# Optimization experiments

Measured on AMD Instinct MI355X. Metric: run time of the kernel, lower is better.

## Reference

```python
import jax, jax.numpy as jnp
import numpy as np

N_NODES = 50000
NEG_SLOPE = 0.2


def _gat_layer(x, src, dst, W, att_src, att_dst, bias, concat):
    # x: [N, F_in]; W: [F_in, H*D]; att_*: [H, D]; bias: [H*D] or [D]
    H, D = att_src.shape
    N = x.shape[0]
    h = (x @ W).reshape(N, H, D)                       # [N, H, D]
    a_s = jnp.einsum('nhd,hd->nh', h, att_src)         # [N, H]
    a_d = jnp.einsum('nhd,hd->nh', h, att_dst)
    e = a_s[src] + a_d[dst]                            # [E, H]
    e = jnp.where(e > 0, e, NEG_SLOPE * e)             # LeakyReLU(0.2)
    # segment softmax over incoming edges of each target node
    e_max = jax.ops.segment_max(e, dst, num_segments=N)
    ex = jnp.exp(e - e_max[dst])
    denom = jax.ops.segment_sum(ex, dst, num_segments=N)
    alpha = ex / denom[dst]                            # [E, H]
    msg = h[src] * alpha[:, :, None]                   # [E, H, D]
    out = jax.ops.segment_sum(msg, dst, num_segments=N)  # [N, H, D]
    if concat:
        out = out.reshape(N, H * D)
    else:
        out = out.mean(axis=1)
    return out + bias


def _forward(x, edge_index, W1, att_src1, att_dst1, b1, W2, att_src2, att_dst2, b2):
    N = x.shape[0]
    loop = jnp.arange(N, dtype=edge_index.dtype)
    src = jnp.concatenate([edge_index[0], loop])       # add self-loops (PyG default)
    dst = jnp.concatenate([edge_index[1], loop])
    h = _gat_layer(x, src, dst, W1, att_src1, att_dst1, b1, concat=True)
    h = jax.nn.elu(h)
    h = _gat_layer(h, src, dst, W2, att_src2, att_dst2, b2, concat=False)
    return jax.nn.log_softmax(h, axis=-1)


def setup_inputs() -> dict:
    key = jax.random.key(0)
    ks = jax.random.split(key, 12)
    N, E, F_in, F_out, H, D = N_NODES, 1600000, 128, 64, 8, 32
    glorot = lambda k, shp: jax.random.normal(k, shp, jnp.float32) * np.sqrt(2.0 / (shp[0] + shp[-1]))
    return {
        'x': jax.random.normal(ks[0], (N, F_in), jnp.float32),
        'edge_index': jax.random.randint(ks[1], (2, E), 0, N, jnp.int64),
        'W1': glorot(ks[2], (F_in, H * D)),
        'att_src1': glorot(ks[3], (H, D)),
        'att_dst1': glorot(ks[4], (H, D)),
        'b1': jnp.zeros((H * D,), jnp.float32),
        'W2': glorot(ks[5], (H * D, F_out)),
        'att_src2': glorot(ks[6], (1, F_out)),
        'att_dst2': glorot(ks[7], (1, F_out)),
        'b2': jnp.zeros((F_out,), jnp.float32),
    }


def reference(x, edge_index, W1, att_src1, att_dst1, b1, W2, att_src2, att_dst2, b2):
    return _forward(x, edge_index, W1, att_src1, att_dst1, b1, W2, att_src2, att_dst2, b2)
```

## Files before the change

### kernel.cpp

```cpp
#include <hip/hip_runtime.h>
#include <hip/hip_bf16.h>
#include <math.h>


#define FIN 128
#define C1 256
#define NH 8
#define HD 32
#define C2 64
#define CH1 64

typedef float floatx2 __attribute__((ext_vector_type(2)));
typedef short bf16x8 __attribute__((ext_vector_type(8)));
typedef float f32x4 __attribute__((ext_vector_type(4)));

__device__ __forceinline__ float blo(unsigned u) { return __uint_as_float(u << 16); }
__device__ __forceinline__ float bhi(unsigned u) { return __uint_as_float(u & 0xffff0000u); }
__device__ __forceinline__ unsigned pkbf(float a, float b) {
    unsigned ua = __float_as_uint(a), ub = __float_as_uint(b);
    ua += 0x7fff + ((ua >> 16) & 1);
    ub += 0x7fff + ((ub >> 16) & 1);
    return (ua >> 16) | (ub & 0xffff0000u);
}

__global__ void zero_kernel(int* p, int n) {
    int i = blockIdx.x * 256 + threadIdx.x;
    if (i < n) p[i] = 0;
}

__global__ void hist_kernel(const int* __restrict__ ei, int E, int ETOT, int T,
                            int* cnt, int* __restrict__ offs) {
    int base = blockIdx.x * 256 + threadIdx.x;
    if (base >= T) return;
    int d[8], o[8];
    #pragma unroll
    for (int i = 0; i < 8; ++i) {
        int e = base + i * T;
        d[i] = (e < ETOT) ? ((e < E) ? ei[E + e] : (e - E)) : -1;
    }
    #pragma unroll
    for (int i = 0; i < 8; ++i)
        if (d[i] >= 0) o[i] = atomicAdd(&cnt[d[i]], 1);
    #pragma unroll
    for (int i = 0; i < 8; ++i)
        if (d[i] >= 0) offs[base + i * T] = o[i];
}

__global__ void scan1_kernel(const int* __restrict__ cnt, int n,
                             int* __restrict__ pref, int* __restrict__ bsum) {
    int tid = threadIdx.x, lane = tid & 63, w = tid >> 6;
    int i = blockIdx.x * 256 + tid;
    int v = (i < n) ? cnt[i] : 0;
    int sc = v;
    #pragma unroll
    for (int d = 1; d < 64; d <<= 1) {
        int t = __shfl_up(sc, d, 64);
        if (lane >= d) sc += t;
    }
    __shared__ int ws[4];
    if (lane == 63) ws[w] = sc;
    __syncthreads();
    int woff = 0;
    #pragma unroll
    for (int k = 0; k < 4; ++k) woff += (k < w) ? ws[k] : 0;
    if (i < n) pref[i] = woff + sc - v;
    if (tid == 255) bsum[blockIdx.x] = woff + sc;
}

__global__ void scan2_kernel(int* bsum, int nb) {
    int tid = threadIdx.x, lane = tid & 63, w = tid >> 6;
    int v = (tid < nb) ? bsum[tid] : 0;
    int sc = v;
    #pragma unroll
    for (int d = 1; d < 64; d <<= 1) {
        int t = __shfl_up(sc, d, 64);
        if (lane >= d) sc += t;
    }
    __shared__ int ws[4];
    if (lane == 63) ws[w] = sc;
    __syncthreads();
    int woff = 0;
    #pragma unroll
    for (int k = 0; k < 4; ++k) woff += (k < w) ? ws[k] : 0;
    __syncthreads();
    if (tid < nb) bsum[tid] = woff + sc - v;
}

__global__ void scan3_kernel(const int* __restrict__ pref, const int* __restrict__ bsum,
                             int n, int ETOT, int* __restrict__ rowptr) {
    int i = blockIdx.x * 256 + threadIdx.x;
    if (i < n) rowptr[i] = pref[i] + bsum[blockIdx.x];
    if (i == 0) rowptr[n] = ETOT;
}

__global__ void scatter_kernel(const int* __restrict__ ei, const int* __restrict__ rowptr,
                               const int* __restrict__ offs, int E, int ETOT, int T,
                               int* __restrict__ colb) {
    int base = blockIdx.x * 256 + threadIdx.x;
    if (base >= T) return;
    #pragma unroll
    for (int i = 0; i < 8; ++i) {
        int e = base + i * T;
        if (e >= ETOT) continue;
        int src, dst;
        if (e < E) { src = ei[e]; dst = ei[E + e]; }
        else       { src = e - E; dst = e - E; }
        colb[rowptr[dst] + offs[e]] = src;
    }
}

__global__ void cvt_x_kernel(const float* __restrict__ x, unsigned* __restrict__ xb, int total8) {
    int i = blockIdx.x * 256 + threadIdx.x;
    if (i >= total8) return;
    const float4* p = reinterpret_cast<const float4*>(x + (size_t)i * 8);
    float4 v0 = p[0], v1 = p[1];
    uint4 o;
    o.x = pkbf(v0.x, v0.y); o.y = pkbf(v0.z, v0.w);
    o.z = pkbf(v1.x, v1.y); o.w = pkbf(v1.z, v1.w);
    reinterpret_cast<uint4*>(xb)[i] = o;
}

__global__ void cvt_w1_kernel(const float* __restrict__ W1, unsigned short* __restrict__ w1t) {
    int k = blockIdx.x, j = threadIdx.x;
    float v = W1[k * C1 + j];
    w1t[j * FIN + k] = (unsigned short)(pkbf(v, v) & 0xffffu);
}

__global__ void cvt_w2_kernel(const float* __restrict__ W2, unsigned short* __restrict__ w2t) {
    int j = blockIdx.x, k = threadIdx.x;
    float v = W2[k * C2 + j];
    w2t[j * C1 + k] = (unsigned short)(pkbf(v, v) & 0xffffu);
}

__global__ __launch_bounds__(256) void gemm1_mfma(
    const unsigned short* __restrict__ xb, const unsigned short* __restrict__ w1t,
    unsigned char* __restrict__ h1, int Nn) {
    __shared__ __align__(16) unsigned char sA[64 * 256];
    int tid = threadIdx.x;
    int row0 = blockIdx.x * 64;
    #pragma unroll
    for (int rep = 0; rep < 4; ++rep) {
        int flat = rep * 256 + tid;
        int row = flat >> 4, c16 = flat & 15;
        uint4 v = make_uint4(0u, 0u, 0u, 0u);
        if (row0 + row < Nn)
            v = *reinterpret_cast<const uint4*>(
                reinterpret_cast<const unsigned char*>(xb) + (size_t)(row0 + row) * 256 + c16 * 16);
        *reinterpret_cast<uint4*>(sA + ((row * 256 + c16 * 16) ^ ((row & 7) << 4))) = v;
    }
    __syncthreads();
    int w = tid >> 6, l = tid & 63;
    int lr = l & 15, lq = l >> 4;
    int arow = w * 16 + lr;
    bf16x8 a[4];
    #pragma unroll
    for (int ks = 0; ks < 4; ++ks)
        a[ks] = *reinterpret_cast<const bf16x8*>(
            sA + ((arow * 256 + ks * 64 + lq * 16) ^ ((arow & 7) << 4)));
    const unsigned char* wb = reinterpret_cast<const unsigned char*>(w1t);
    #pragma unroll
    for (int nt = 0; nt < 16; ++nt) {
        f32x4 acc = {0.f, 0.f, 0.f, 0.f};
        #pragma unroll
        for (int ks = 0; ks < 4; ++ks) {
            bf16x8 b = *reinterpret_cast<const bf16x8*>(
                wb + (size_t)(nt * 16 + lr) * 256 + ks * 64 + lq * 16);
            acc = __builtin_amdgcn_mfma_f32_16x16x32_bf16(a[ks], b, acc, 0, 0, 0);
        }
        int col = nt * 16 + lr;
        #pragma unroll
        for (int reg = 0; reg < 4; ++reg) {
            int row = row0 + w * 16 + lq * 4 + reg;
            if (row < Nn) {
                unsigned pk = __builtin_amdgcn_cvt_pk_fp8_f32(acc[reg], acc[reg], 0, false);
                h1[(size_t)row * C1 + col] = (unsigned char)(pk & 0xffu);
            }
        }
    }
}

__global__ __launch_bounds__(256) void att1_kernel(
    const unsigned char* __restrict__ h1, const float* __restrict__ att_s,
    const float* __restrict__ att_d, float* __restrict__ as1, float* __restrict__ ad1, int Nn) {
    int tid = threadIdx.x;
    int row = blockIdx.x * 16 + (tid >> 4);
    int l16 = tid & 15;
    if (row >= Nn) return;
    uint4 u = *reinterpret_cast<const uint4*>(h1 + (size_t)row * C1 + l16 * 16);
    float hv[16];
    unsigned uu[4] = {u.x, u.y, u.z, u.w};
    #pragma unroll
    for (int q = 0; q < 4; ++q) {
        floatx2 f0 = __builtin_amdgcn_cvt_pk_f32_fp8((int)uu[q], false);
        floatx2 f1 = __builtin_amdgcn_cvt_pk_f32_fp8((int)uu[q], true);
        hv[q * 4 + 0] = f0.x; hv[q * 4 + 1] = f0.y;
        hv[q * 4 + 2] = f1.x; hv[q * 4 + 3] = f1.y;
    }
    int col0 = l16 * 16;
    const float4* asp = reinterpret_cast<const float4*>(att_s + col0);
    const float4* adp = reinterpret_cast<const float4*>(att_d + col0);
    float ps = 0.f, pd = 0.f;
    #pragma unroll
    for (int q = 0; q < 4; ++q) {
        float4 sa = asp[q], da = adp[q];
        ps += hv[q*4+0]*sa.x + hv[q*4+1]*sa.y + hv[q*4+2]*sa.z + hv[q*4+3]*sa.w;
        pd += hv[q*4+0]*da.x + hv[q*4+1]*da.y + hv[q*4+2]*da.z + hv[q*4+3]*da.w;
    }
    ps += __shfl_xor(ps, 1, 64);
    pd += __shfl_xor(pd, 1, 64);
    if ((l16 & 1) == 0) {
        as1[row * NH + (l16 >> 1)] = ps;
        ad1[row * NH + (l16 >> 1)] = pd;
    }
}

__global__ __launch_bounds__(256) void agg1_kernel(
    const int* __restrict__ rowptr, const int* __restrict__ colb,
    const float* __restrict__ as1, const float* __restrict__ ad1,
    const unsigned char* __restrict__ h1, const float* __restrict__ b1,
    __hip_bfloat16* __restrict__ x1e, int N) {
    int wid = threadIdx.x >> 6, lane = threadIdx.x & 63;
    int n = blockIdx.x * 4 + wid;
    __shared__ float sp[4][CH1 * 9];
    __shared__ int ssrc[4][CH1];
    __shared__ float advs[4][NH];
    if (n >= N) return;
    int start = rowptr[n], end = rowptr[n + 1];
    int h = lane >> 3, sub = lane & 7;
    int half = lane >> 5, l5 = lane & 31;
    int hq = l5 >> 2;
    ssrc[wid][lane] = 0;
    if (lane < NH) advs[wid][lane] = ad1[n * NH + lane];
    float adr[NH];
    #pragma unroll
    for (int hh = 0; hh < NH; ++hh) adr[hh] = advs[wid][hh];

    float m = -INFINITY, denom = 0.f;
    floatx2 A01 = {0.f, 0.f}, A23 = {0.f, 0.f}, A45 = {0.f, 0.f}, A67 = {0.f, 0.f};
    for (int base = start; base < end; base += CH1) {
        int cn = min(CH1, end - base);
        if (lane < cn) {
            int s = colb[base + lane];
            ssrc[wid][lane] = s;
            const float4* ap = reinterpret_cast<const float4*>(as1 + (size_t)s * NH);
            float4 q0 = ap[0], q1 = ap[1];
            float av[8] = {q0.x, q0.y, q0.z, q0.w, q1.x, q1.y, q1.z, q1.w};
            #pragma unroll
            for (int hh = 0; hh < NH; ++hh) {
                float e = av[hh] + adr[hh];
                e = e > 0.f ? e : 0.2f * e;
                sp[wid][lane * 9 + hh] = e;
            }
        }
        float cmax = -INFINITY;
        for (int e = sub; e < cn; e += 8) cmax = fmaxf(cmax, sp[wid][e * 9 + h]);
        #pragma unroll
        for (int mk = 4; mk >= 1; mk >>= 1) cmax = fmaxf(cmax, __shfl_xor(cmax, mk, 64));
        float newm = fmaxf(m, cmax);
        float scale = __expf(m - newm);
        float scale_g = __shfl(scale, hq << 3, 64);
        floatx2 s2 = {scale_g, scale_g};
        A01 *= s2; A23 *= s2; A45 *= s2; A67 *= s2;
        denom *= scale; m = newm;
        float psum = 0.f;
        for (int e = sub; e < cn; e += 8) {
            float p = __expf(sp[wid][e * 9 + h] - m);
            sp[wid][e * 9 + h] = p;
            psum += p;
        }
        #pragma unroll
        for (int mk = 4; mk >= 1; mk >>= 1) psum += __shfl_xor(psum, mk, 64);
        denom += psum;
        #pragma unroll 2
        for (int e2 = 0; e2 < cn; e2 += 2) {
            int e = e2 + half;
            bool ok = e < cn;
            int s = ssrc[wid][ok ? e : 0];
            float p = ok ? sp[wid][e * 9 + hq] : 0.f;
            floatx2 p2 = {p, p};
            uint2 u = *reinterpret_cast<const uint2*>(h1 + (size_t)s * C1 + l5 * 8);
            floatx2 f01 = __builtin_amdgcn_cvt_pk_f32_fp8((int)u.x, false);
            floatx2 f23 = __builtin_amdgcn_cvt_pk_f32_fp8((int)u.x, true);
            floatx2 f45 = __builtin_amdgcn_cvt_pk_f32_fp8((int)u.y, false);
            floatx2 f67 = __builtin_amdgcn_cvt_pk_f32_fp8((int)u.y, true);
            A01 = __builtin_elementwise_fma(p2, f01, A01);
            A23 = __builtin_elementwise_fma(p2, f23, A23);
            A45 = __builtin_elementwise_fma(p2, f45, A45);
            A67 = __builtin_elementwise_fma(p2, f67, A67);
        }
    }
    float a0 = A01.x, a1 = A01.y, a2 = A23.x, a3 = A23.y;
    float a4 = A45.x, a5 = A45.y, a6 = A67.x, a7 = A67.y;
    a0 += __shfl_xor(a0, 32, 64); a1 += __shfl_xor(a1, 32, 64);
    a2 += __shfl_xor(a2, 32, 64); a3 += __shfl_xor(a3, 32, 64);
    a4 += __shfl_xor(a4, 32, 64); a5 += __shfl_xor(a5, 32, 64);
    a6 += __shfl_xor(a6, 32, 64); a7 += __shfl_xor(a7, 32, 64);
    float invd = 1.f / __shfl(denom, hq << 3, 64);
    if (half == 0) {
        const float4* bp = reinterpret_cast<const float4*>(b1 + l5 * 8);
        float4 bv0 = bp[0], bv1 = bp[1];
        float v0 = a0 * invd + bv0.x, v1 = a1 * invd + bv0.y;
        float v2 = a2 * invd + bv0.z, v3 = a3 * invd + bv0.w;
        float v4 = a4 * invd + bv1.x, v5 = a5 * invd + bv1.y;
        float v6 = a6 * invd + bv1.z, v7 = a7 * invd + bv1.w;
        v0 = v0 > 0.f ? v0 : __expf(v0) - 1.f;
        v1 = v1 > 0.f ? v1 : __expf(v1) - 1.f;
        v2 = v2 > 0.f ? v2 : __expf(v2) - 1.f;
        v3 = v3 > 0.f ? v3 : __expf(v3) - 1.f;
        v4 = v4 > 0.f ? v4 : __expf(v4) - 1.f;
        v5 = v5 > 0.f ? v5 : __expf(v5) - 1.f;
        v6 = v6 > 0.f ? v6 : __expf(v6) - 1.f;
        v7 = v7 > 0.f ? v7 : __expf(v7) - 1.f;
        uint4 w;
        w.x = pkbf(v0, v1); w.y = pkbf(v2, v3);
        w.z = pkbf(v4, v5); w.w = pkbf(v6, v7);
        *reinterpret_cast<uint4*>(x1e + (size_t)n * C1 + l5 * 8) = w;
    }
}

__global__ __launch_bounds__(256) void gemm2_mfma(
    const unsigned short* __restrict__ x1e, const unsigned short* __restrict__ w2t,
    unsigned short* __restrict__ h2, int Nn) {
    __shared__ __align__(16) unsigned char sA[64 * 512];
    int tid = threadIdx.x;
    int row0 = blockIdx.x * 64;
    #pragma unroll
    for (int rep = 0; rep < 8; ++rep) {
        int flat = rep * 256 + tid;
        int row = flat >> 5, c16 = flat & 31;
        uint4 v = make_uint4(0u, 0u, 0u, 0u);
        if (row0 + row < Nn)
            v = *reinterpret_cast<const uint4*>(
                reinterpret_cast<const unsigned char*>(x1e) + (size_t)(row0 + row) * 512 + c16 * 16);
        *reinterpret_cast<uint4*>(sA + ((row * 512 + c16 * 16) ^ ((row & 7) << 4))) = v;
    }
    __syncthreads();
    int w = tid >> 6, l = tid & 63;
    int lr = l & 15, lq = l >> 4;
    int arow = w * 16 + lr;
    bf16x8 a[8];
    #pragma unroll
    for (int ks = 0; ks < 8; ++ks)
        a[ks] = *reinterpret_cast<const bf16x8*>(
            sA + ((arow * 512 + ks * 64 + lq * 16) ^ ((arow & 7) << 4)));
    const unsigned char* wb = reinterpret_cast<const unsigned char*>(w2t);
    #pragma unroll
    for (int nt = 0; nt < 4; ++nt) {
        f32x4 acc = {0.f, 0.f, 0.f, 0.f};
        #pragma unroll
        for (int ks = 0; ks < 8; ++ks) {
            bf16x8 b = *reinterpret_cast<const bf16x8*>(
                wb + (size_t)(nt * 16 + lr) * 512 + ks * 64 + lq * 16);
            acc = __builtin_amdgcn_mfma_f32_16x16x32_bf16(a[ks], b, acc, 0, 0, 0);
        }
        int col = nt * 16 + lr;
        #pragma unroll
        for (int reg = 0; reg < 4; ++reg) {
            int row = row0 + w * 16 + lq * 4 + reg;
            if (row < Nn)
                h2[(size_t)row * C2 + col] = (unsigned short)(pkbf(acc[reg], acc[reg]) & 0xffffu);
        }
    }
}

__global__ __launch_bounds__(256) void att2_kernel(
    const unsigned short* __restrict__ h2, const float* __restrict__ att_s2,
    const float* __restrict__ att_d2, float* __restrict__ as2, float* __restrict__ ad2, int Nn) {
    int tid = threadIdx.x;
    int row = blockIdx.x * 16 + (tid >> 4);
    int l16 = tid & 15;
    if (row >= Nn) return;
    uint2 u = *reinterpret_cast<const uint2*>(h2 + (size_t)row * C2 + l16 * 4);
    float h0 = blo(u.x), h1v = bhi(u.x), h2v = blo(u.y), h3 = bhi(u.y);
    const float4* asp = reinterpret_cast<const float4*>(att_s2 + l16 * 4);
    const float4* adp = reinterpret_cast<const float4*>(att_d2 + l16 * 4);
    float4 sa = asp[0], da = adp[0];
    float ps = h0*sa.x + h1v*sa.y + h2v*sa.z + h3*sa.w;
    float pd = h0*da.x + h1v*da.y + h2v*da.z + h3*da.w;
    #pragma unroll
    for (int mk = 8; mk >= 1; mk >>= 1) {
        ps += __shfl_xor(ps, mk, 64);
        pd += __shfl_xor(pd, mk, 64);
    }
    if (l16 == 0) { as2[row] = ps; ad2[row] = pd; }
}

__global__ __launch_bounds__(256) void agg2_kernel(
    const int* __restrict__ rowptr, const int* __restrict__ colb,
    const float* __restrict__ as2, const float* __restrict__ ad2,
    const __hip_bfloat16* __restrict__ h2, const float* __restrict__ b2,
    float* __restrict__ out, int N) {
    int wid = threadIdx.x >> 6, lane = threadIdx.x & 63;
    int n = blockIdx.x * 4 + wid;
    __shared__ float sp2[4][64];
    __shared__ int ssrc2[4][64];
    if (n >= N) return;
    int start = rowptr[n], end = rowptr[n + 1];
    int q = lane >> 4, l4 = lane & 15;
    ssrc2[wid][lane] = 0;
    float adn = ad2[n];
    float m = -INFINITY, denom = 0.f;
    floatx2 A01 = {0.f, 0.f}, A23 = {0.f, 0.f};
    for (int base = start; base < end; base += 64) {
        int cn = min(64, end - base);
        float logit = -INFINITY;
        if (lane < cn) {
            int s = colb[base + lane];
            ssrc2[wid][lane] = s;
            float e = as2[s] + adn;
            logit = e > 0.f ? e : 0.2f * e;
        }
        float cmax = logit;
        #pragma unroll
        for (int mk = 32; mk >= 1; mk >>= 1) cmax = fmaxf(cmax, __shfl_xor(cmax, mk, 64));
        float newm = fmaxf(m, cmax);
        float scale = __expf(m - newm);
        floatx2 s2 = {scale, scale};
        A01 *= s2; A23 *= s2;
        denom *= scale; m = newm;
        float p = (lane < cn) ? __expf(logit - m) : 0.f;
        sp2[wid][lane] = p;
        float psum = p;
        #pragma unroll
        for (int mk = 32; mk >= 1; mk >>= 1) psum += __shfl_xor(psum, mk, 64);
        denom += psum;
        #pragma unroll 2
        for (int e2 = 0; e2 < cn; e2 += 4) {
            int e = e2 + q;
            bool ok = e < cn;
            int s = ssrc2[wid][ok ? e : 0];
            float pe = ok ? sp2[wid][e] : 0.f;
            floatx2 p2 = {pe, pe};
            uint2 u = *reinterpret_cast<const uint2*>(h2 + (size_t)s * C2 + l4 * 4);
            floatx2 f01 = {blo(u.x), bhi(u.x)};
            floatx2 f23 = {blo(u.y), bhi(u.y)};
            A01 = __builtin_elementwise_fma(p2, f01, A01);
            A23 = __builtin_elementwise_fma(p2, f23, A23);
        }
    }
    float a0 = A01.x, a1 = A01.y, a2 = A23.x, a3 = A23.y;
    a0 += __shfl_xor(a0, 16, 64); a1 += __shfl_xor(a1, 16, 64);
    a2 += __shfl_xor(a2, 16, 64); a3 += __shfl_xor(a3, 16, 64);
    a0 += __shfl_xor(a0, 32, 64); a1 += __shfl_xor(a1, 32, 64);
    a2 += __shfl_xor(a2, 32, 64); a3 += __shfl_xor(a3, 32, 64);
    float invd = 1.f / denom;
    const float4* bp = reinterpret_cast<const float4*>(b2 + l4 * 4);
    float4 bv = bp[0];
    float v0 = a0 * invd + bv.x, v1 = a1 * invd + bv.y;
    float v2 = a2 * invd + bv.z, v3 = a3 * invd + bv.w;
    float mx = fmaxf(fmaxf(v0, v1), fmaxf(v2, v3));
    #pragma unroll
    for (int mk = 8; mk >= 1; mk >>= 1) mx = fmaxf(mx, __shfl_xor(mx, mk, 64));
    float sum = __expf(v0 - mx) + __expf(v1 - mx) + __expf(v2 - mx) + __expf(v3 - mx);
    #pragma unroll
    for (int mk = 8; mk >= 1; mk >>= 1) sum += __shfl_xor(sum, mk, 64);
    float ls = logf(sum);
    if (q == 0) {
        float4 o = make_float4(v0 - mx - ls, v1 - mx - ls, v2 - mx - ls, v3 - mx - ls);
        *reinterpret_cast<float4*>(out + (size_t)n * C2 + l4 * 4) = o;
    }
}

extern "C" void kernel_launch(void* const* d_in, const int* in_sizes, int n_in,
                              void* d_out, int out_size, void* d_ws, size_t ws_size,
                              hipStream_t stream) {
    const float* x      = (const float*)d_in[0];
    const int*   ei     = (const int*)d_in[1];
    const float* W1     = (const float*)d_in[2];
    const float* att_s1 = (const float*)d_in[3];
    const float* att_d1 = (const float*)d_in[4];
    const float* b1     = (const float*)d_in[5];
    const float* W2     = (const float*)d_in[6];
    const float* att_s2 = (const float*)d_in[7];
    const float* att_d2 = (const float*)d_in[8];
    const float* b2     = (const float*)d_in[9];
    float* out = (float*)d_out;

    const int N = out_size / C2;
    const int E = in_sizes[1] / 2;
    const int ETOT = E + N;
    const int NB = (N + 255) / 256;

    char* ws = (char*)d_ws;
    size_t off = 0;
    auto alloc = [&](size_t bytes) -> void* {
        void* p = ws + off;
        off += (bytes + 255) & ~(size_t)255;
        return p;
    };
    unsigned char* h1 = (unsigned char*)alloc((size_t)N * C1);
    __hip_bfloat16* x1e = (__hip_bfloat16*)alloc((size_t)N * C1 * 2);
    unsigned* xb = (unsigned*)alloc((size_t)N * FIN * 2);
    unsigned short* w1t = (unsigned short*)alloc((size_t)C1 * FIN * 2);
    unsigned short* w2t = (unsigned short*)alloc((size_t)C2 * C1 * 2);
    float* as1  = (float*)alloc((size_t)N * NH * 4);
    float* ad1  = (float*)alloc((size_t)N * NH * 4);
    float* as2  = (float*)alloc((size_t)N * 4);
    float* ad2  = (float*)alloc((size_t)N * 4);
    int*   cnt    = (int*)alloc((size_t)N * 4);
    int*   rowptr = (int*)alloc((size_t)(N + 1) * 4);
    int*   pref   = (int*)alloc((size_t)N * 4);
    int*   bsum   = (int*)alloc((size_t)NB * 4);
    int*   offs   = (int*)alloc((size_t)ETOT * 4);
    int*   colb   = (int*)alloc((size_t)ETOT * 4);
    unsigned short* h2 = (unsigned short*)h1;

    const int T = (ETOT + 7) / 8;
    zero_kernel<<<(N + 255) / 256, 256, 0, stream>>>(cnt, N);
    hist_kernel<<<(T + 255) / 256, 256, 0, stream>>>(ei, E, ETOT, T, cnt, offs);
    scan1_kernel<<<NB, 256, 0, stream>>>(cnt, N, pref, bsum);
    scan2_kernel<<<1, 256, 0, stream>>>(bsum, NB);
    scan3_kernel<<<NB, 256, 0, stream>>>(pref, bsum, N, ETOT, rowptr);
    scatter_kernel<<<(T + 255) / 256, 256, 0, stream>>>(ei, rowptr, offs, E, ETOT, T, colb);

    int total8 = N * FIN / 8;
    cvt_x_kernel<<<(total8 + 255) / 256, 256, 0, stream>>>(x, xb, total8);
    cvt_w1_kernel<<<FIN, C1, 0, stream>>>(W1, w1t);
    cvt_w2_kernel<<<C2, C1, 0, stream>>>(W2, w2t);

    gemm1_mfma<<<(N + 63) / 64, 256, 0, stream>>>((const unsigned short*)xb, w1t, h1, N);
    att1_kernel<<<(N + 15) / 16, 256, 0, stream>>>(h1, att_s1, att_d1, as1, ad1, N);
    agg1_kernel<<<(N + 3) / 4, 256, 0, stream>>>(rowptr, colb, as1, ad1, h1, b1, x1e, N);

    gemm2_mfma<<<(N + 63) / 64, 256, 0, stream>>>((const unsigned short*)x1e, w2t, h2, N);
    att2_kernel<<<(N + 15) / 16, 256, 0, stream>>>(h2, att_s2, att_d2, as2, ad2, N);
    agg2_kernel<<<(N + 3) / 4, 256, 0, stream>>>(rowptr, colb, as2, ad2,
                                                 (const __hip_bfloat16*)h2, b2, out, N);
}
```

Measured before the change: 301.8 us.

## Fuse attention logits into GEMM epilogues, merge conversion kernels, shrink agg blocks

The attention-score dot products (as/ad) are now computed in the MFMA GEMM epilogues from full-precision accumulators, which removes the separate att1/att2 kernels and their re-read of h1/h2. The three conversion kernels are merged into one prep launch. The aggregation kernels drop to 2 waves per block and keep precomputed byte offsets in shared memory. The edge hist/scatter kernels process 4 edges per thread instead of 8. The attention logits now come from fp32 values rather than the quantized fp8/bf16 stored features, which shifts numerics slightly, and the epilogue adds shuffle work inside the GEMM.

```diff
diff --git a/kernel.cpp b/kernel.cpp
--- a/kernel.cpp
+++ b/kernel.cpp
@@ -32,17 +32,17 @@
                             int* cnt, int* __restrict__ offs) {
     int base = blockIdx.x * 256 + threadIdx.x;
     if (base >= T) return;
-    int d[8], o[8];
-    #pragma unroll
-    for (int i = 0; i < 8; ++i) {
+    int d[4], o[4];
+    #pragma unroll
+    for (int i = 0; i < 4; ++i) {
         int e = base + i * T;
         d[i] = (e < ETOT) ? ((e < E) ? ei[E + e] : (e - E)) : -1;
     }
     #pragma unroll
-    for (int i = 0; i < 8; ++i)
+    for (int i = 0; i < 4; ++i)
         if (d[i] >= 0) o[i] = atomicAdd(&cnt[d[i]], 1);
     #pragma unroll
-    for (int i = 0; i < 8; ++i)
+    for (int i = 0; i < 4; ++i)
         if (d[i] >= 0) offs[base + i * T] = o[i];
 }
 
@@ -99,7 +99,7 @@
     int base = blockIdx.x * 256 + threadIdx.x;
     if (base >= T) return;
     #pragma unroll
-    for (int i = 0; i < 8; ++i) {
+    for (int i = 0; i < 4; ++i) {
         int e = base + i * T;
         if (e >= ETOT) continue;
         int src, dst;
@@ -109,32 +109,39 @@
     }
 }
 
-__global__ void cvt_x_kernel(const float* __restrict__ x, unsigned* __restrict__ xb, int total8) {
+__global__ void prep_kernel(const float* __restrict__ x, const float* __restrict__ W1,
+                            const float* __restrict__ W2, unsigned* __restrict__ xb,
+                            unsigned short* __restrict__ w1t, unsigned short* __restrict__ w2t,
+                            int total8) {
     int i = blockIdx.x * 256 + threadIdx.x;
-    if (i >= total8) return;
-    const float4* p = reinterpret_cast<const float4*>(x + (size_t)i * 8);
-    float4 v0 = p[0], v1 = p[1];
-    uint4 o;
-    o.x = pkbf(v0.x, v0.y); o.y = pkbf(v0.z, v0.w);
-    o.z = pkbf(v1.x, v1.y); o.w = pkbf(v1.z, v1.w);
-    reinterpret_cast<uint4*>(xb)[i] = o;
-}
-
-__global__ void cvt_w1_kernel(const float* __restrict__ W1, unsigned short* __restrict__ w1t) {
-    int k = blockIdx.x, j = threadIdx.x;
-    float v = W1[k * C1 + j];
-    w1t[j * FIN + k] = (unsigned short)(pkbf(v, v) & 0xffffu);
-}
-
-__global__ void cvt_w2_kernel(const float* __restrict__ W2, unsigned short* __restrict__ w2t) {
-    int j = blockIdx.x, k = threadIdx.x;
-    float v = W2[k * C2 + j];
-    w2t[j * C1 + k] = (unsigned short)(pkbf(v, v) & 0xffffu);
+    if (i < total8) {
+        const float4* p = reinterpret_cast<const float4*>(x + (size_t)i * 8);
+        float4 v0 = p[0], v1 = p[1];
+        uint4 o;
+        o.x = pkbf(v0.x, v0.y); o.y = pkbf(v0.z, v0.w);
+        o.z = pkbf(v1.x, v1.y); o.w = pkbf(v1.z, v1.w);
+        reinterpret_cast<uint4*>(xb)[i] = o;
+        return;
+    }
+    int j1 = i - total8;
+    if (j1 < C1 * FIN) {
+        int j = j1 >> 7, k = j1 & 127;
+        float v = W1[(size_t)k * C1 + j];
+        w1t[j1] = (unsigned short)(pkbf(v, v) & 0xffffu);
+        return;
+    }
+    int j2 = j1 - C1 * FIN;
+    if (j2 < C2 * C1) {
+        int j = j2 >> 8, k = j2 & 255;
+        float v = W2[(size_t)k * C2 + j];
+        w2t[j2] = (unsigned short)(pkbf(v, v) & 0xffffu);
+    }
 }
 
 __global__ __launch_bounds__(256) void gemm1_mfma(
     const unsigned short* __restrict__ xb, const unsigned short* __restrict__ w1t,
-    unsigned char* __restrict__ h1, int Nn) {
+    const float* __restrict__ att_s, const float* __restrict__ att_d,
+    unsigned char* __restrict__ h1, float* __restrict__ as1, float* __restrict__ ad1, int Nn) {
     __shared__ __align__(16) unsigned char sA[64 * 256];
     int tid = threadIdx.x;
     int row0 = blockIdx.x * 64;
@@ -158,6 +165,7 @@
         a[ks] = *reinterpret_cast<const bf16x8*>(
             sA + ((arow * 256 + ks * 64 + lq * 16) ^ ((arow & 7) << 4)));
     const unsigned char* wb = reinterpret_cast<const unsigned char*>(w1t);
+    float ps[4] = {0.f, 0.f, 0.f, 0.f}, pd[4] = {0.f, 0.f, 0.f, 0.f};
     #pragma unroll
     for (int nt = 0; nt < 16; ++nt) {
         f32x4 acc = {0.f, 0.f, 0.f, 0.f};
@@ -168,6 +176,7 @@
             acc = __builtin_amdgcn_mfma_f32_16x16x32_bf16(a[ks], b, acc, 0, 0, 0);
         }
         int col = nt * 16 + lr;
+        float sa = att_s[col], da = att_d[col];
         #pragma unroll
         for (int reg = 0; reg < 4; ++reg) {
             int row = row0 + w * 16 + lq * 4 + reg;
@@ -175,61 +184,51 @@
                 unsigned pk = __builtin_amdgcn_cvt_pk_fp8_f32(acc[reg], acc[reg], 0, false);
                 h1[(size_t)row * C1 + col] = (unsigned char)(pk & 0xffu);
             }
-        }
-    }
-}
-
-__global__ __launch_bounds__(256) void att1_kernel(
-    const unsigned char* __restrict__ h1, const float* __restrict__ att_s,
-    const float* __restrict__ att_d, float* __restrict__ as1, float* __restrict__ ad1, int Nn) {
-    int tid = threadIdx.x;
-    int row = blockIdx.x * 16 + (tid >> 4);
-    int l16 = tid & 15;
-    if (row >= Nn) return;
-    uint4 u = *reinterpret_cast<const uint4*>(h1 + (size_t)row * C1 + l16 * 16);
-    float hv[16];
-    unsigned uu[4] = {u.x, u.y, u.z, u.w};
-    #pragma unroll
-    for (int q = 0; q < 4; ++q) {
-        floatx2 f0 = __builtin_amdgcn_cvt_pk_f32_fp8((int)uu[q], false);
-        floatx2 f1 = __builtin_amdgcn_cvt_pk_f32_fp8((int)uu[q], true);
-        hv[q * 4 + 0] = f0.x; hv[q * 4 + 1] = f0.y;
-        hv[q * 4 + 2] = f1.x; hv[q * 4 + 3] = f1.y;
-    }
-    int col0 = l16 * 16;
-    const float4* asp = reinterpret_cast<const float4*>(att_s + col0);
-    const float4* adp = reinterpret_cast<const float4*>(att_d + col0);
-    float ps = 0.f, pd = 0.f;
-    #pragma unroll
-    for (int q = 0; q < 4; ++q) {
-        float4 sa = asp[q], da = adp[q];
-        ps += hv[q*4+0]*sa.x + hv[q*4+1]*sa.y + hv[q*4+2]*sa.z + hv[q*4+3]*sa.w;
-        pd += hv[q*4+0]*da.x + hv[q*4+1]*da.y + hv[q*4+2]*da.z + hv[q*4+3]*da.w;
-    }
-    ps += __shfl_xor(ps, 1, 64);
-    pd += __shfl_xor(pd, 1, 64);
-    if ((l16 & 1) == 0) {
-        as1[row * NH + (l16 >> 1)] = ps;
-        ad1[row * NH + (l16 >> 1)] = pd;
-    }
-}
-
-__global__ __launch_bounds__(256) void agg1_kernel(
+            ps[reg] = fmaf(acc[reg], sa, ps[reg]);
+            pd[reg] = fmaf(acc[reg], da, pd[reg]);
+        }
+        if (nt & 1) {
+            #pragma unroll
+            for (int reg = 0; reg < 4; ++reg) {
+                #pragma unroll
+                for (int mk = 8; mk >= 1; mk >>= 1) {
+                    ps[reg] += __shfl_xor(ps[reg], mk, 64);
+                    pd[reg] += __shfl_xor(pd[reg], mk, 64);
+                }
+            }
+            if (lr == 0) {
+                int hh = nt >> 1;
+                #pragma unroll
+                for (int reg = 0; reg < 4; ++reg) {
+                    int row = row0 + w * 16 + lq * 4 + reg;
+                    if (row < Nn) {
+                        as1[row * NH + hh] = ps[reg];
+                        ad1[row * NH + hh] = pd[reg];
+                    }
+                }
+            }
+            #pragma unroll
+            for (int reg = 0; reg < 4; ++reg) { ps[reg] = 0.f; pd[reg] = 0.f; }
+        }
+    }
+}
+
+__global__ __launch_bounds__(128) void agg1_kernel(
     const int* __restrict__ rowptr, const int* __restrict__ colb,
     const float* __restrict__ as1, const float* __restrict__ ad1,
     const unsigned char* __restrict__ h1, const float* __restrict__ b1,
     __hip_bfloat16* __restrict__ x1e, int N) {
     int wid = threadIdx.x >> 6, lane = threadIdx.x & 63;
-    int n = blockIdx.x * 4 + wid;
-    __shared__ float sp[4][CH1 * 9];
-    __shared__ int ssrc[4][CH1];
-    __shared__ float advs[4][NH];
+    int n = blockIdx.x * 2 + wid;
+    __shared__ float sp[2][CH1 * 9];
+    __shared__ int soff[2][CH1];
+    __shared__ float advs[2][NH];
     if (n >= N) return;
     int start = rowptr[n], end = rowptr[n + 1];
     int h = lane >> 3, sub = lane & 7;
     int half = lane >> 5, l5 = lane & 31;
     int hq = l5 >> 2;
-    ssrc[wid][lane] = 0;
+    soff[wid][lane & 63] = 0;
     if (lane < NH) advs[wid][lane] = ad1[n * NH + lane];
     float adr[NH];
     #pragma unroll
@@ -241,7 +240,7 @@
         int cn = min(CH1, end - base);
         if (lane < cn) {
             int s = colb[base + lane];
-            ssrc[wid][lane] = s;
+            soff[wid][lane] = s << 8;
             const float4* ap = reinterpret_cast<const float4*>(as1 + (size_t)s * NH);
             float4 q0 = ap[0], q1 = ap[1];
             float av[8] = {q0.x, q0.y, q0.z, q0.w, q1.x, q1.y, q1.z, q1.w};
@@ -275,10 +274,10 @@
         for (int e2 = 0; e2 < cn; e2 += 2) {
             int e = e2 + half;
             bool ok = e < cn;
-            int s = ssrc[wid][ok ? e : 0];
+            int off = soff[wid][ok ? e : 0];
             float p = ok ? sp[wid][e * 9 + hq] : 0.f;
             floatx2 p2 = {p, p};
-            uint2 u = *reinterpret_cast<const uint2*>(h1 + (size_t)s * C1 + l5 * 8);
+            uint2 u = *reinterpret_cast<const uint2*>(h1 + off + l5 * 8);
             floatx2 f01 = __builtin_amdgcn_cvt_pk_f32_fp8((int)u.x, false);
             floatx2 f23 = __builtin_amdgcn_cvt_pk_f32_fp8((int)u.x, true);
             floatx2 f45 = __builtin_amdgcn_cvt_pk_f32_fp8((int)u.y, false);
@@ -320,7 +319,8 @@
 
 __global__ __launch_bounds__(256) void gemm2_mfma(
     const unsigned short* __restrict__ x1e, const unsigned short* __restrict__ w2t,
-    unsigned short* __restrict__ h2, int Nn) {
+    const float* __restrict__ att_s2, const float* __restrict__ att_d2,
+    unsigned short* __restrict__ h2, float* __restrict__ as2, float* __restrict__ ad2, int Nn) {
     __shared__ __align__(16) unsigned char sA[64 * 512];
     int tid = threadIdx.x;
     int row0 = blockIdx.x * 64;
@@ -344,6 +344,7 @@
         a[ks] = *reinterpret_cast<const bf16x8*>(
             sA + ((arow * 512 + ks * 64 + lq * 16) ^ ((arow & 7) << 4)));
     const unsigned char* wb = reinterpret_cast<const unsigned char*>(w2t);
+    float ps[4] = {0.f, 0.f, 0.f, 0.f}, pd[4] = {0.f, 0.f, 0.f, 0.f};
     #pragma unroll
     for (int nt = 0; nt < 4; ++nt) {
         f32x4 acc = {0.f, 0.f, 0.f, 0.f};
@@ -354,50 +355,46 @@
             acc = __builtin_amdgcn_mfma_f32_16x16x32_bf16(a[ks], b, acc, 0, 0, 0);
         }
         int col = nt * 16 + lr;
+        float sa = att_s2[col], da = att_d2[col];
         #pragma unroll
         for (int reg = 0; reg < 4; ++reg) {
             int row = row0 + w * 16 + lq * 4 + reg;
             if (row < Nn)
                 h2[(size_t)row * C2 + col] = (unsigned short)(pkbf(acc[reg], acc[reg]) & 0xffffu);
-        }
-    }
-}
-
-__global__ __launch_bounds__(256) void att2_kernel(
-    const unsigned short* __restrict__ h2, const float* __restrict__ att_s2,
-    const float* __restrict__ att_d2, float* __restrict__ as2, float* __restrict__ ad2, int Nn) {
-    int tid = threadIdx.x;
-    int row = blockIdx.x * 16 + (tid >> 4);
-    int l16 = tid & 15;
-    if (row >= Nn) return;
-    uint2 u = *reinterpret_cast<const uint2*>(h2 + (size_t)row * C2 + l16 * 4);
-    float h0 = blo(u.x), h1v = bhi(u.x), h2v = blo(u.y), h3 = bhi(u.y);
-    const float4* asp = reinterpret_cast<const float4*>(att_s2 + l16 * 4);
-    const float4* adp = reinterpret_cast<const float4*>(att_d2 + l16 * 4);
-    float4 sa = asp[0], da = adp[0];
-    float ps = h0*sa.x + h1v*sa.y + h2v*sa.z + h3*sa.w;
-    float pd = h0*da.x + h1v*da.y + h2v*da.z + h3*da.w;
-    #pragma unroll
-    for (int mk = 8; mk >= 1; mk >>= 1) {
-        ps += __shfl_xor(ps, mk, 64);
-        pd += __shfl_xor(pd, mk, 64);
-    }
-    if (l16 == 0) { as2[row] = ps; ad2[row] = pd; }
-}
-
-__global__ __launch_bounds__(256) void agg2_kernel(
+            ps[reg] = fmaf(acc[reg], sa, ps[reg]);
+            pd[reg] = fmaf(acc[reg], da, pd[reg]);
+        }
+    }
+    #pragma unroll
+    for (int reg = 0; reg < 4; ++reg) {
+        #pragma unroll
+        for (int mk = 8; mk >= 1; mk >>= 1) {
+            ps[reg] += __shfl_xor(ps[reg], mk, 64);
+            pd[reg] += __shfl_xor(pd[reg], mk, 64);
+        }
+    }
+    if (lr == 0) {
+        #pragma unroll
+        for (int reg = 0; reg < 4; ++reg) {
+            int row = row0 + w * 16 + lq * 4 + reg;
+            if (row < Nn) { as2[row] = ps[reg]; ad2[row] = pd[reg]; }
+        }
+    }
+}
+
+__global__ __launch_bounds__(128) void agg2_kernel(
     const int* __restrict__ rowptr, const int* __restrict__ colb,
     const float* __restrict__ as2, const float* __restrict__ ad2,
     const __hip_bfloat16* __restrict__ h2, const float* __restrict__ b2,
     float* __restrict__ out, int N) {
     int wid = threadIdx.x >> 6, lane = threadIdx.x & 63;
-    int n = blockIdx.x * 4 + wid;
-    __shared__ float sp2[4][64];
-    __shared__ int ssrc2[4][64];
+    int n = blockIdx.x * 2 + wid;
+    __shared__ float sp2[2][64];
+    __shared__ int soff2[2][64];
     if (n >= N) return;
     int start = rowptr[n], end = rowptr[n + 1];
     int q = lane >> 4, l4 = lane & 15;
-    ssrc2[wid][lane] = 0;
+    soff2[wid][lane] = 0;
     float adn = ad2[n];
     float m = -INFINITY, denom = 0.f;
     floatx2 A01 = {0.f, 0.f}, A23 = {0.f, 0.f};
@@ -406,7 +403,7 @@
         float logit = -INFINITY;
         if (lane < cn) {
             int s = colb[base + lane];
-            ssrc2[wid][lane] = s;
+            soff2[wid][lane] = s << 7;
             float e = as2[s] + adn;
             logit = e > 0.f ? e : 0.2f * e;
         }
@@ -428,10 +425,11 @@
         for (int e2 = 0; e2 < cn; e2 += 4) {
             int e = e2 + q;
             bool ok = e < cn;
-            int s = ssrc2[wid][ok ? e : 0];
+            int off = soff2[wid][ok ? e : 0];
             float pe = ok ? sp2[wid][e] : 0.f;
             floatx2 p2 = {pe, pe};
-            uint2 u = *reinterpret_cast<const uint2*>(h2 + (size_t)s * C2 + l4 * 4);
+            uint2 u = *reinterpret_cast<const uint2*>(
+                reinterpret_cast<const unsigned char*>(h2) + off + l4 * 8);
             floatx2 f01 = {blo(u.x), bhi(u.x)};
             floatx2 f23 = {blo(u.y), bhi(u.y)};
             A01 = __builtin_elementwise_fma(p2, f01, A01);
@@ -505,7 +503,7 @@
     int*   colb   = (int*)alloc((size_t)ETOT * 4);
     unsigned short* h2 = (unsigned short*)h1;
 
-    const int T = (ETOT + 7) / 8;
+    const int T = (ETOT + 3) / 4;
     zero_kernel<<<(N + 255) / 256, 256, 0, stream>>>(cnt, N);
     hist_kernel<<<(T + 255) / 256, 256, 0, stream>>>(ei, E, ETOT, T, cnt, offs);
     scan1_kernel<<<NB, 256, 0, stream>>>(cnt, N, pref, bsum);
@@ -514,16 +512,15 @@
     scatter_kernel<<<(T + 255) / 256, 256, 0, stream>>>(ei, rowptr, offs, E, ETOT, T, colb);
 
     int total8 = N * FIN / 8;
-    cvt_x_kernel<<<(total8 + 255) / 256, 256, 0, stream>>>(x, xb, total8);
-    cvt_w1_kernel<<<FIN, C1, 0, stream>>>(W1, w1t);
-    cvt_w2_kernel<<<C2, C1, 0, stream>>>(W2, w2t);
-
-    gemm1_mfma<<<(N + 63) / 64, 256, 0, stream>>>((const unsigned short*)xb, w1t, h1, N);
-    att1_kernel<<<(N + 15) / 16, 256, 0, stream>>>(h1, att_s1, att_d1, as1, ad1, N);
-    agg1_kernel<<<(N + 3) / 4, 256, 0, stream>>>(rowptr, colb, as1, ad1, h1, b1, x1e, N);
-
-    gemm2_mfma<<<(N + 63) / 64, 256, 0, stream>>>((const unsigned short*)x1e, w2t, h2, N);
-    att2_kernel<<<(N + 15) / 16, 256, 0, stream>>>(h2, att_s2, att_d2, as2, ad2, N);
-    agg2_kernel<<<(N + 3) / 4, 256, 0, stream>>>(rowptr, colb, as2, ad2,
+    int prep_total = total8 + C1 * FIN + C2 * C1;
+    prep_kernel<<<(prep_total + 255) / 256, 256, 0, stream>>>(x, W1, W2, xb, w1t, w2t, total8);
+
+    gemm1_mfma<<<(N + 63) / 64, 256, 0, stream>>>((const unsigned short*)xb, w1t,
+                                                  att_s1, att_d1, h1, as1, ad1, N);
+    agg1_kernel<<<(N + 1) / 2, 128, 0, stream>>>(rowptr, colb, as1, ad1, h1, b1, x1e, N);
+
+    gemm2_mfma<<<(N + 63) / 64, 256, 0, stream>>>((const unsigned short*)x1e, w2t,
+                                                  att_s2, att_d2, h2, as2, ad2, N);
+    agg2_kernel<<<(N + 1) / 2, 128, 0, stream>>>(rowptr, colb, as2, ad2,
                                                  (const __hip_bfloat16*)h2, b2, out, N);
 }
```

Result: faster. 285.8 us (-5.3%).
